# Optimization experiments

Hardware: AMD Instinct MI355X
Metric: run time of the kernel (lower is better)

Reference implementation:

```python
import jax, jax.numpy as jnp
import numpy as np

B, T, I, H, O = 256, 1024, 128, 256, 64


def setup_inputs() -> dict:
    key = jax.random.key(0)
    ks = jax.random.split(key, 8)
    s_ih = 1.0 / np.sqrt(H)
    return {
        "x": jax.random.normal(ks[0], (B, T, I), dtype=jnp.float32),
        "W_ih": jax.random.normal(ks[1], (3 * H, I), dtype=jnp.float32) * s_ih,
        "W_hh": jax.random.normal(ks[2], (3 * H, H), dtype=jnp.float32) * s_ih,
        "b_ih": jax.random.normal(ks[3], (3 * H,), dtype=jnp.float32) * s_ih,
        "b_hh": jax.random.normal(ks[4], (3 * H,), dtype=jnp.float32) * s_ih,
        "alpha": jax.random.normal(ks[5], (H,), dtype=jnp.float32),
        "fc_w": jax.random.normal(ks[6], (O, H), dtype=jnp.float32) * s_ih,
        "fc_b": jax.random.normal(ks[7], (O,), dtype=jnp.float32) * s_ih,
    }


def _pagru_last_hidden(x, W_ih, W_hh, b_ih, b_hh, alpha):
    # Precompute all input-side gate projections in one big GEMM: [T, B, 3H]
    xg = jnp.einsum("bti,gi->tbg", x, W_ih) + b_ih
    a = jax.nn.sigmoid(alpha)  # per-unit adaptive interpolation gate

    def step(h, gi):
        gh = h @ W_hh.T + b_hh                      # [B, 3H]
        i_r, i_z, i_n = jnp.split(gi, 3, axis=-1)
        h_r, h_z, h_n = jnp.split(gh, 3, axis=-1)
        r = jax.nn.sigmoid(i_r + h_r)
        z = jax.nn.sigmoid(i_z + h_z)
        n = jnp.tanh(i_n + r * h_n)
        h_new = (1.0 - z) * n + z * h               # torch GRUCell convention
        h_out = a * h_new + (1.0 - a) * h           # parameter-adaptive update
        return h_out, None

    h0 = jnp.zeros((x.shape[0], W_hh.shape[1]), dtype=x.dtype)
    h_last, _ = jax.lax.scan(step, h0, xg)
    return h_last


def reference(x, W_ih, W_hh, b_ih, b_hh, alpha, fc_w, fc_b):
    h_last = _pagru_last_hidden(x, W_ih, W_hh, b_ih, b_hh, alpha)
    return jax.nn.sigmoid(h_last @ fc_w.T + fc_b)   # [B, O]
```

## Files before the change

kernel.cpp:

```cpp
#include <hip/hip_runtime.h>
#include <cstdint>
#include <cstddef>

#define TT 1024
#define BB 256
#define II 128
#define HH 256
#define GG 768
#define OO 64
#define TCH 256
#define NCH (TT / TCH)

typedef float f32x4 __attribute__((ext_vector_type(4)));
typedef short short8 __attribute__((ext_vector_type(8)));

__device__ __forceinline__ unsigned f2bf(float f) {
  unsigned u = __builtin_bit_cast(unsigned, f);
  return (u + 0x7FFFu + ((u >> 16) & 1u)) >> 16;
}
__device__ __forceinline__ float bflo(unsigned p) {
  return __builtin_bit_cast(float, p << 16);
}
__device__ __forceinline__ float bfhi(unsigned p) {
  return __builtin_bit_cast(float, p & 0xffff0000u);
}
__device__ __forceinline__ unsigned cvtpk_bf16(float lo, float hi) {
  unsigned r;
  asm("v_cvt_pk_bf16_f32 %0, %1, %2" : "=v"(r) : "v"(lo), "v"(hi));
  return r;
}
__device__ __forceinline__ float sigm(float x) {
  return __builtin_amdgcn_rcpf(1.f + __builtin_amdgcn_exp2f(-1.44269504088896f * x));
}

__global__ void k_btot(const float* __restrict__ bih, const float* __restrict__ bhh,
                       float* __restrict__ btot) {
  int i = blockIdx.x * 256 + threadIdx.x;
  if (i < GG) btot[i] = bih[i] + (i < 512 ? bhh[i] : 0.f);
}

__global__ __attribute__((amdgpu_flat_work_group_size(512, 512), amdgpu_waves_per_eu(2, 2)))
void k_xg(const float* __restrict__ x,
    const float* __restrict__ Wih, const float* __restrict__ btot,
    unsigned short* __restrict__ xg, int t0)
{
  __shared__ unsigned short xlds[BB * II];
  const int tid = threadIdx.x;
  const int tl = blockIdx.x;
  const int tg = t0 + tl;
  const int w = tid >> 6, lane = tid & 63, cu = lane & 15, quad = lane >> 4;

  for (int i = 0; i < 16; ++i) {
    int cid = tid + i * 512;
    int row = cid >> 5, c16 = cid & 31;
    const float4 v = *(const float4*)(x + (size_t)row * TT * II + (size_t)tg * II + c16 * 4);
    unsigned lo = f2bf(v.x) | (f2bf(v.y) << 16);
    unsigned hi = f2bf(v.z) | (f2bf(v.w) << 16);
    int byt = (row * 256 + c16 * 8) ^ ((row & 7) << 4);
    *(uint2*)((char*)xlds + byt) = make_uint2(lo, hi);
  }

  uint4 WA[3][2][4];
  float bias[3][2][4];
  #pragma unroll
  for (int pp = 0; pp < 3; ++pp)
    #pragma unroll
    for (int t2 = 0; t2 < 2; ++t2) {
      int ut = w * 6 + pp * 2 + t2;
      int grow = ut * 16 + cu;
      const float4* wr = (const float4*)(Wih + (size_t)grow * II);
      #pragma unroll
      for (int kk = 0; kk < 4; ++kk) {
        float4 lo = wr[kk * 8 + quad * 2];
        float4 hi = wr[kk * 8 + quad * 2 + 1];
        uint4 pk;
        pk.x = f2bf(lo.x) | (f2bf(lo.y) << 16);
        pk.y = f2bf(lo.z) | (f2bf(lo.w) << 16);
        pk.z = f2bf(hi.x) | (f2bf(hi.y) << 16);
        pk.w = f2bf(hi.z) | (f2bf(hi.w) << 16);
        WA[pp][t2][kk] = pk;
      }
      #pragma unroll
      for (int j = 0; j < 4; ++j)
        bias[pp][t2][j] = btot[ut * 16 + quad * 4 + j];
    }
  __syncthreads();

  #pragma unroll 1
  for (int mt = 0; mt < 16; ++mt) {
    short8 bf[4];
    int brow = mt * 16 + cu;
    #pragma unroll
    for (int kk = 0; kk < 4; ++kk) {
      int byt = (brow * 256 + kk * 64 + quad * 16) ^ ((cu & 7) << 4);
      bf[kk] = *(const short8*)((const char*)xlds + byt);
    }
    f32x4 acc[3][2];
    #pragma unroll
    for (int pp = 0; pp < 3; ++pp) {
      acc[pp][0] = (f32x4){0.f, 0.f, 0.f, 0.f};
      acc[pp][1] = (f32x4){0.f, 0.f, 0.f, 0.f};
    }
    #pragma unroll
    for (int kk = 0; kk < 4; ++kk)
      #pragma unroll
      for (int pp = 0; pp < 3; ++pp)
        #pragma unroll
        for (int t2 = 0; t2 < 2; ++t2)
          acc[pp][t2] = __builtin_amdgcn_mfma_f32_16x16x32_bf16(
              __builtin_bit_cast(short8, WA[pp][t2][kk]), bf[kk], acc[pp][t2], 0, 0, 0);
    #pragma unroll
    for (int pp = 0; pp < 3; ++pp)
      #pragma unroll
      for (int t2 = 0; t2 < 2; ++t2) {
        int ut = w * 6 + pp * 2 + t2;
        unsigned p0 = cvtpk_bf16(acc[pp][t2][0] + bias[pp][t2][0],
                                 acc[pp][t2][1] + bias[pp][t2][1]);
        unsigned p1 = cvtpk_bf16(acc[pp][t2][2] + bias[pp][t2][2],
                                 acc[pp][t2][3] + bias[pp][t2][3]);
        size_t rec = ((size_t)(tl * 16 + mt) * 48 + ut) * 64 + lane;
        ((uint2*)xg)[rec] = make_uint2(p0, p1);
      }
  }
}

__global__ __launch_bounds__(1024, 4) void k_scan(const float* __restrict__ Whh,
    const float* __restrict__ bhh, const float* __restrict__ alpha,
    const unsigned short* __restrict__ xg, float* __restrict__ hlast, int t0)
{
  __shared__ unsigned short hbuf[2][16 * 256];
  __shared__ uint4 wlds[16][3][64];
  const int tid = threadIdx.x, wv = tid >> 6, lane = tid & 63;
  const int cu = lane & 15, quad = lane >> 4;
  const int wg = blockIdx.x;

  uint4 Wf[3][7];
  #pragma unroll
  for (int g = 0; g < 3; ++g) {
    int grow = g * 256 + wv * 16 + cu;
    const float4* wr = (const float4*)(Whh + (size_t)grow * HH);
    #pragma unroll
    for (int kk = 0; kk < 8; ++kk) {
      float4 lo = wr[kk * 8 + quad * 2];
      float4 hi = wr[kk * 8 + quad * 2 + 1];
      uint4 pk;
      pk.x = cvtpk_bf16(lo.x, lo.y);
      pk.y = cvtpk_bf16(lo.z, lo.w);
      pk.z = cvtpk_bf16(hi.x, hi.y);
      pk.w = cvtpk_bf16(hi.z, hi.w);
      if (kk < 7) Wf[g][kk] = pk;
      else        wlds[wv][g][lane] = pk;
    }
  }
  const int u0 = wv * 16 + quad * 4;
  unsigned asigp[2], bhp[2];
  asigp[0] = cvtpk_bf16(sigm(alpha[u0]),     sigm(alpha[u0 + 1]));
  asigp[1] = cvtpk_bf16(sigm(alpha[u0 + 2]), sigm(alpha[u0 + 3]));
  bhp[0] = f2bf(bhh[512 + u0])     | (f2bf(bhh[512 + u0 + 1]) << 16);
  bhp[1] = f2bf(bhh[512 + u0 + 2]) | (f2bf(bhh[512 + u0 + 3]) << 16);

  for (int i = 0; i < 4; ++i) {
    int idx = tid * 4 + i;
    int m = idx >> 8, u = idx & 255;
    float hv = (t0 == 0) ? 0.f : hlast[((size_t)wg * 16 + m) * 256 + u];
    int byt = (m * 512 + u * 2) ^ ((m & 7) << 4);
    *(unsigned short*)((char*)hbuf[0] + byt) = (unsigned short)f2bf(hv);
  }
  __syncthreads();

  const unsigned vb  = (unsigned)((cu * 512 + quad * 16) ^ ((cu & 7) << 4));
  const unsigned whp = (unsigned)((cu * 512 + wv * 32 + quad * 8) ^ ((cu & 7) << 4));

  const uint2* xq = (const uint2*)xg + ((size_t)wg * 48 + wv) * 64 + lane;
  uint2 qn0 = xq[0], qn1 = xq[1024], qn2 = xq[2048];

  unsigned bufb = 0;
  const char* hbase = (const char*)hbuf;

  for (int tl = 0; tl < TCH; ++tl) {
    const char* hs = hbase + bufb;
    f32x4 acc[3];
    acc[0][0]=bflo(qn0.x); acc[0][1]=bfhi(qn0.x); acc[0][2]=bflo(qn0.y); acc[0][3]=bfhi(qn0.y);
    acc[1][0]=bflo(qn1.x); acc[1][1]=bfhi(qn1.x); acc[1][2]=bflo(qn1.y); acc[1][3]=bfhi(qn1.y);
    acc[2][0]=bflo(bhp[0]); acc[2][1]=bfhi(bhp[0]);
    acc[2][2]=bflo(bhp[1]); acc[2][3]=bfhi(bhp[1]);
    uint2 q2c = qn2;
    if (tl < TCH - 1) xq += 49152;
    qn0 = xq[0]; qn1 = xq[1024]; qn2 = xq[2048];
    uint2 hpq = *(const uint2*)(hs + whp);

    #pragma unroll
    for (int kk = 0; kk < 7; ++kk) {
      short8 bfh = *(const short8*)(hs + (vb ^ (unsigned)(kk * 64)));
      #pragma unroll
      for (int g = 0; g < 3; ++g)
        acc[g] = __builtin_amdgcn_mfma_f32_16x16x32_bf16(
            __builtin_bit_cast(short8, Wf[g][kk]), bfh, acc[g], 0, 0, 0);
    }
    {
      short8 bfh = *(const short8*)(hs + (vb ^ (unsigned)(7 * 64)));
      #pragma unroll
      for (int g = 0; g < 3; ++g) {
        short8 wf = __builtin_bit_cast(short8, wlds[wv][g][lane]);
        acc[g] = __builtin_amdgcn_mfma_f32_16x16x32_bf16(wf, bfh, acc[g], 0, 0, 0);
      }
    }

    float hpv[4] = {bflo(hpq.x), bfhi(hpq.x), bflo(hpq.y), bfhi(hpq.y)};
    float xgn[4] = {bflo(q2c.x), bfhi(q2c.x), bflo(q2c.y), bfhi(q2c.y)};
    float av[4]  = {bflo(asigp[0]), bfhi(asigp[0]), bflo(asigp[1]), bfhi(asigp[1])};
    float ho[4];
    #pragma unroll
    for (int j = 0; j < 4; ++j) {
      float rr = sigm(acc[0][j]);
      float ss = sigm(-acc[1][j]);
      float v  = fmaf(rr, acc[2][j], xgn[j]);
      float nn = 1.f - 2.f * __builtin_amdgcn_rcpf(
                     1.f + __builtin_amdgcn_exp2f(2.88539008177793f * v));
      ho[j] = fmaf(av[j] * ss, nn - hpv[j], hpv[j]);
    }
    unsigned p0 = cvtpk_bf16(ho[0], ho[1]);
    unsigned p1 = cvtpk_bf16(ho[2], ho[3]);
    *(uint2*)((char*)hbase + (bufb ^ 8192u) + whp) = make_uint2(p0, p1);
    if (tl == TCH - 1) {
      #pragma unroll
      for (int j = 0; j < 4; ++j)
        hlast[((size_t)wg * 16 + cu) * 256 + u0 + j] = ho[j];
    }
    __syncthreads();
    bufb ^= 8192u;
  }
}

__global__ void k_out(const float* __restrict__ hlast, const float* __restrict__ fcw,
                      const float* __restrict__ fcb, float* __restrict__ out)
{
  int g = blockIdx.x * 256 + threadIdx.x;
  int b = g >> 6, o = g & 63;
  const float* hr = hlast + (size_t)b * HH;
  const float* wr = fcw + (size_t)o * HH;
  float acc = fcb[o];
  for (int u = 0; u < HH; ++u) acc = fmaf(hr[u], wr[u], acc);
  out[g] = sigm(acc);
}

extern "C" void kernel_launch(void* const* d_in, const int* in_sizes, int n_in,
                              void* d_out, int out_size, void* d_ws, size_t ws_size,
                              hipStream_t stream)
{
  const float* x   = (const float*)d_in[0];
  const float* Wih = (const float*)d_in[1];
  const float* Whh = (const float*)d_in[2];
  const float* bih = (const float*)d_in[3];
  const float* bhh = (const float*)d_in[4];
  const float* alp = (const float*)d_in[5];
  const float* fcw = (const float*)d_in[6];
  const float* fcb = (const float*)d_in[7];
  float* out = (float*)d_out;

  const size_t XGB   = (size_t)TCH * 16 * 48 * 64 * 8;
  const size_t HLB   = (size_t)BB * HH * 4;
  const size_t BTB   = (size_t)GG * 4;
  if (ws_size < XGB + HLB + BTB) return;

  unsigned short* xg = (unsigned short*)d_ws;
  float* hlast = (float*)((char*)d_ws + XGB);
  float* btot  = (float*)((char*)d_ws + XGB + HLB);

  k_btot<<<3, 256, 0, stream>>>(bih, bhh, btot);
  for (int c = 0; c < NCH; ++c) {
    k_xg  <<<TCH, 512, 0, stream>>>(x, Wih, btot, xg, c * TCH);
    k_scan<<<16, 1024, 0, stream>>>(Whh, bhh, alp, xg, hlast, c * TCH);
  }
  k_out<<<64, 256, 0, stream>>>(hlast, fcw, fcb, out);
}
```

Before: 1.657 ms.

## Stream pre-packed bf16 W_hh slices from global each step instead of holding them in registers

A new pre-pass kernel packs W_hh into the bf16 MFMA fragment layout once, in workspace. The scan kernel now keeps only two k-slices per gate in registers and one in LDS. The remaining five slices are reloaded from global memory (L2-resident) every timestep through a two-slot double buffer. This cuts register pressure, but it puts global loads on the serial recurrence critical path, and the time chunk is also halved, doubling the kernel launches.

```diff
diff --git a/kernel.cpp b/kernel.cpp
--- a/kernel.cpp
+++ b/kernel.cpp
@@ -8,7 +8,7 @@
 #define HH 256
 #define GG 768
 #define OO 64
-#define TCH 256
+#define TCH 128
 #define NCH (TT / TCH)
 
 typedef float f32x4 __attribute__((ext_vector_type(4)));
@@ -37,6 +37,24 @@
                        float* __restrict__ btot) {
   int i = blockIdx.x * 256 + threadIdx.x;
   if (i < GG) btot[i] = bih[i] + (i < 512 ? bhh[i] : 0.f);
+}
+
+__global__ void k_wpack(const float* __restrict__ Whh, uint4* __restrict__ wpk) {
+  const int ut = blockIdx.x;
+  const int lane = threadIdx.x;
+  const int cu = lane & 15, quad = lane >> 4;
+  const float4* wr = (const float4*)(Whh + (size_t)(ut * 16 + cu) * HH);
+  #pragma unroll
+  for (int kk = 0; kk < 8; ++kk) {
+    float4 lo = wr[kk * 8 + quad * 2];
+    float4 hi = wr[kk * 8 + quad * 2 + 1];
+    uint4 pk;
+    pk.x = cvtpk_bf16(lo.x, lo.y);
+    pk.y = cvtpk_bf16(lo.z, lo.w);
+    pk.z = cvtpk_bf16(hi.x, hi.y);
+    pk.w = cvtpk_bf16(hi.z, hi.w);
+    wpk[(ut * 8 + kk) * 64 + lane] = pk;
+  }
 }
 
 __global__ __attribute__((amdgpu_flat_work_group_size(512, 512), amdgpu_waves_per_eu(2, 2)))
@@ -124,9 +142,10 @@
   }
 }
 
-__global__ __launch_bounds__(1024, 4) void k_scan(const float* __restrict__ Whh,
+__global__ __launch_bounds__(1024, 4) void k_scan(
     const float* __restrict__ bhh, const float* __restrict__ alpha,
-    const unsigned short* __restrict__ xg, float* __restrict__ hlast, int t0)
+    const uint4* __restrict__ wpk, const unsigned short* __restrict__ xg,
+    float* __restrict__ hlast, int t0)
 {
   __shared__ unsigned short hbuf[2][16 * 256];
   __shared__ uint4 wlds[16][3][64];
@@ -134,24 +153,22 @@
   const int cu = lane & 15, quad = lane >> 4;
   const int wg = blockIdx.x;
 
-  uint4 Wf[3][7];
+  const uint4* wbase = wpk + lane;
+  uint4 Wf[3][2];
   #pragma unroll
   for (int g = 0; g < 3; ++g) {
-    int grow = g * 256 + wv * 16 + cu;
-    const float4* wr = (const float4*)(Whh + (size_t)grow * HH);
-    #pragma unroll
-    for (int kk = 0; kk < 8; ++kk) {
-      float4 lo = wr[kk * 8 + quad * 2];
-      float4 hi = wr[kk * 8 + quad * 2 + 1];
-      uint4 pk;
-      pk.x = cvtpk_bf16(lo.x, lo.y);
-      pk.y = cvtpk_bf16(lo.z, lo.w);
-      pk.z = cvtpk_bf16(hi.x, hi.y);
-      pk.w = cvtpk_bf16(hi.z, hi.w);
-      if (kk < 7) Wf[g][kk] = pk;
-      else        wlds[wv][g][lane] = pk;
-    }
-  }
+    #pragma unroll
+    for (int kk = 0; kk < 2; ++kk)
+      Wf[g][kk] = wbase[((g * 16 + wv) * 8 + kk) * 64];
+    wlds[wv][g][lane] = wbase[((g * 16 + wv) * 8 + 2) * 64];
+  }
+  uint4 sbuf[2][3];
+  #pragma unroll
+  for (int g = 0; g < 3; ++g) {
+    sbuf[1][g] = wbase[((g * 16 + wv) * 8 + 3) * 64];
+    sbuf[0][g] = wbase[((g * 16 + wv) * 8 + 4) * 64];
+  }
+
   const int u0 = wv * 16 + quad * 4;
   unsigned asigp[2], bhp[2];
   asigp[0] = cvtpk_bf16(sigm(alpha[u0]),     sigm(alpha[u0 + 1]));
@@ -190,19 +207,28 @@
     uint2 hpq = *(const uint2*)(hs + whp);
 
     #pragma unroll
-    for (int kk = 0; kk < 7; ++kk) {
+    for (int kk = 0; kk < 8; ++kk) {
       short8 bfh = *(const short8*)(hs + (vb ^ (unsigned)(kk * 64)));
-      #pragma unroll
-      for (int g = 0; g < 3; ++g)
-        acc[g] = __builtin_amdgcn_mfma_f32_16x16x32_bf16(
-            __builtin_bit_cast(short8, Wf[g][kk]), bfh, acc[g], 0, 0, 0);
-    }
-    {
-      short8 bfh = *(const short8*)(hs + (vb ^ (unsigned)(7 * 64)));
-      #pragma unroll
-      for (int g = 0; g < 3; ++g) {
-        short8 wf = __builtin_bit_cast(short8, wlds[wv][g][lane]);
-        acc[g] = __builtin_amdgcn_mfma_f32_16x16x32_bf16(wf, bfh, acc[g], 0, 0, 0);
+      if (kk < 2) {
+        #pragma unroll
+        for (int g = 0; g < 3; ++g)
+          acc[g] = __builtin_amdgcn_mfma_f32_16x16x32_bf16(
+              __builtin_bit_cast(short8, Wf[g][kk]), bfh, acc[g], 0, 0, 0);
+      } else if (kk == 2) {
+        #pragma unroll
+        for (int g = 0; g < 3; ++g) {
+          short8 wf = __builtin_bit_cast(short8, wlds[wv][g][lane]);
+          acc[g] = __builtin_amdgcn_mfma_f32_16x16x32_bf16(wf, bfh, acc[g], 0, 0, 0);
+        }
+      } else {
+        #pragma unroll
+        for (int g = 0; g < 3; ++g)
+          acc[g] = __builtin_amdgcn_mfma_f32_16x16x32_bf16(
+              __builtin_bit_cast(short8, sbuf[kk & 1][g]), bfh, acc[g], 0, 0, 0);
+        const int s = (kk >= 6) ? (10 - kk) : (kk + 2);
+        #pragma unroll
+        for (int g = 0; g < 3; ++g)
+          sbuf[s & 1][g] = wbase[((g * 16 + wv) * 8 + s) * 64];
       }
     }
 
@@ -258,19 +284,22 @@
   const float* fcb = (const float*)d_in[7];
   float* out = (float*)d_out;
 
-  const size_t XGB   = (size_t)TCH * 16 * 48 * 64 * 8;
-  const size_t HLB   = (size_t)BB * HH * 4;
-  const size_t BTB   = (size_t)GG * 4;
-  if (ws_size < XGB + HLB + BTB) return;
+  const size_t XGB = (size_t)TCH * 16 * 48 * 64 * 8;
+  const size_t HLB = (size_t)BB * HH * 4;
+  const size_t BTB = (size_t)GG * 4;
+  const size_t WPB = (size_t)48 * 8 * 64 * 16;
+  if (ws_size < XGB + HLB + BTB + WPB) return;
 
   unsigned short* xg = (unsigned short*)d_ws;
   float* hlast = (float*)((char*)d_ws + XGB);
   float* btot  = (float*)((char*)d_ws + XGB + HLB);
-
-  k_btot<<<3, 256, 0, stream>>>(bih, bhh, btot);
+  uint4* wpk   = (uint4*)((char*)d_ws + XGB + HLB + BTB);
+
+  k_btot <<<3, 256, 0, stream>>>(bih, bhh, btot);
+  k_wpack<<<48, 64, 0, stream>>>(Whh, wpk);
   for (int c = 0; c < NCH; ++c) {
     k_xg  <<<TCH, 512, 0, stream>>>(x, Wih, btot, xg, c * TCH);
-    k_scan<<<16, 1024, 0, stream>>>(Whh, bhh, alp, xg, hlast, c * TCH);
+    k_scan<<<16, 1024, 0, stream>>>(bhh, alp, wpk, xg, hlast, c * TCH);
   }
   k_out<<<64, 256, 0, stream>>>(hlast, fcw, fcb, out);
 }
```

After: 2.223 ms. 1.34x slower.
